# Performance work log

Hardware: AMD Instinct MI355X
Metric: run time of the kernel (lower is better)

The kernel has to match this reference:

```python
import jax, jax.numpy as jnp
import numpy as np


def setup_inputs() -> dict:
    key = jax.random.key(0)
    k1, k2 = jax.random.split(key)
    B, C, H, W = 8, 256, 128, 128
    x = jax.random.normal(k1, (B, C, H, W), dtype=jnp.float32)
    # prior plays the role of torch.rand initial selection score (shape [B, H*W])
    prior = jax.random.uniform(k2, (B, H * W), dtype=jnp.float32)
    return {"x": x, "prior": prior, "nbVec": 16}


def reference(x, prior, nbVec):
    # representativeVectors(x, nbVec, prior=prior, onlySimSample=True, applyUMAP=False)
    B, C, H, W = x.shape
    N = H * W
    xf = x.transpose(0, 2, 3, 1).reshape(B, N, C)  # [B, N, C]
    batch = jnp.arange(B)
    EPS = 1e-12  # numerical guard for sqrt at the selected point (dist == 0)

    def step(carry, i):
        score, selpos = carry  # score: [B, N] selection score, selpos: [B, N]
        # i == 0: deterministic center pick; else data-dependent argmax of score
        ind = jnp.where(i == 0, N // 2, jnp.argmax(score, axis=1))  # [B]
        selpos = selpos.at[batch, ind].add(1.0)
        rv = xf[batch, ind]  # gathered representative candidates [B, C]
        # exp(-euclidean_dist / 20) similarity to every spatial position
        d = jnp.sqrt(jnp.sum((xf - rv[:, None, :]) ** 2, axis=-1) + EPS)  # [B, N]
        sim = jnp.exp(-d / 20.0)
        simNorm = sim / jnp.sum(sim, axis=1, keepdims=True)
        repr_vec = jnp.einsum('bnc,bn->bc', xf, simNorm)  # weighted reduction
        score = jnp.where(i == 0, 1.0 - sim, (1.0 - sim) * score)
        return (score, selpos), (repr_vec, sim)

    init = (prior, jnp.zeros((B, N), dtype=x.dtype))
    (_, selpos), (reprVecs, sims) = jax.lax.scan(step, init, jnp.arange(nbVec))
    # reprVecs: [nbVec, B, C]; sims -> [nbVec, B, 1, H, W]; selpos -> [B, 1, H, W]
    return reprVecs, sims.reshape(nbVec, B, 1, H, W), selpos.reshape(B, 1, H, W)
```

## Files before the change

### kernel.cpp

```cpp
#include <hip/hip_runtime.h>
#include <math.h>

#define BB 8
#define CC 256
#define HH 128
#define WW 128
#define NN (HH*WW)
#define NBVEC 16
#define CSPLIT 16
#define CCHUNK (CC/CSPLIT)
#define NBX (NN/256)
#define NBB 16
#define NSUB 4


__global__ __launch_bounds__(256, 8)
void fused_kernel(const float* __restrict__ x,
                  float* __restrict__ out,
                  const double* __restrict__ bmaxv,
                  const int* __restrict__ bmaxi,
                  float* __restrict__ d2part,
                  double* __restrict__ wpart, int iter)
{
    const int b  = blockIdx.z;
    const int cz = blockIdx.y;
    const int nb = blockIdx.x;
    const int t  = threadIdx.x;

    __shared__ float s_x[CCHUNK][257];
    __shared__ float s_sim[256];
    __shared__ float s_rv[CCHUNK];
    __shared__ union UScratch {
        double part[16][CCHUNK];
        struct { double val[NBX]; int idx[NBX]; } mx;
    } s_u;

    float* out_sims   = out + (size_t)NBVEC*BB*CC;
    float* out_selpos = out_sims + (size_t)NBVEC*BB*NN;

    const float* xb   = x + ((size_t)b*CC + (size_t)cz*CCHUNK)*NN + (size_t)nb*(NSUB*256);
    const float* simb = out_sims + (size_t)(iter-1)*BB*NN + (size_t)b*NN + (size_t)nb*(NSUB*256);
    float r[CCHUNK];
    #pragma unroll
    for (int c = 0; c < CCHUNK; ++c)
        r[c] = xb[(size_t)c*NN + t];
    float simreg = 0.0f;
    if (iter > 0) simreg = simb[t];

    int sel = NN/2;
    if (iter > 0 && iter < NBVEC) {
        if (t < NBX) { s_u.mx.val[t] = bmaxv[b*NBX + t]; s_u.mx.idx[t] = bmaxi[b*NBX + t]; }
        __syncthreads();
        for (int s = NBX/2; s > 0; s >>= 1) {
            if (t < s) {
                double v2 = s_u.mx.val[t+s]; int i2 = s_u.mx.idx[t+s];
                if (v2 > s_u.mx.val[t] || (v2 == s_u.mx.val[t] && i2 < s_u.mx.idx[t])) {
                    s_u.mx.val[t] = v2; s_u.mx.idx[t] = i2;
                }
            }
            __syncthreads();
        }
        sel = s_u.mx.idx[0];
    }

    if (iter < NBVEC) {
        if (t < CCHUNK)
            s_rv[t] = x[((size_t)b*CC + (size_t)cz*CCHUNK + t)*NN + sel];
        if (t == 0 && nb == 0 && cz == 0)
            out_selpos[(size_t)b*NN + sel] += 1.0f;
    }

    for (int sub = 0; sub < NSUB; ++sub) {
        __syncthreads();
        #pragma unroll
        for (int c = 0; c < CCHUNK; ++c)
            s_x[c][t] = r[c];
        if (iter > 0) s_sim[t] = simreg;
        __syncthreads();

        if (sub + 1 < NSUB) {
            const int off = (sub+1)*256;
            #pragma unroll
            for (int c = 0; c < CCHUNK; ++c)
                r[c] = xb[(size_t)c*NN + off + t];
            if (iter > 0) simreg = simb[off + t];
        }

        const int n = nb*(NSUB*256) + sub*256 + t;

        if (iter < NBVEC) {
            double acc = 0.0;
            #pragma unroll
            for (int c = 0; c < CCHUNK; ++c) {
                double diff = (double)s_x[c][t] - (double)s_rv[c];
                acc = fma(diff, diff, acc);
            }
            d2part[((size_t)cz*BB + b)*NN + n] = (float)acc;
        }

        if (iter > 0) {
            const int c = t & 15;
            const int g = t >> 4;
            double w = 0.0;
            #pragma unroll
            for (int k = 0; k < 16; ++k) {
                const int nn2 = g*16 + k;
                w = fma((double)s_sim[nn2], (double)s_x[c][nn2], w);
            }
            s_u.part[g][c] = w;
            __syncthreads();
            if (t < CCHUNK) {
                double t0 = 0.0, t1 = 0.0;
                #pragma unroll
                for (int gg = 0; gg < 16; gg += 2) {
                    t0 += s_u.part[gg][t];
                    t1 += s_u.part[gg+1][t];
                }
                const int nbg = nb*NSUB + sub;
                wpart[((size_t)nbg*BB + b)*CC + (size_t)cz*CCHUNK + t] = t0 + t1;
            }
        }
    }
}

__global__ void finish_kernel(float* __restrict__ out,
                              double* __restrict__ score,
                              const float* __restrict__ d2part,
                              double* __restrict__ sumSim,
                              const double* __restrict__ wpart,
                              double* __restrict__ bmaxv,
                              int* __restrict__ bmaxi, int iter)
{
    const int b = blockIdx.y;
    const int t = threadIdx.x;
    const int n = blockIdx.x * 256 + t;
    const size_t si = (size_t)b*NN + n;
    const int lane = t & 63;
    const int wave = t >> 6;

    double a0 = 0.0, a1 = 0.0;
    #pragma unroll
    for (int cz = 0; cz < CSPLIT; cz += 2) {
        a0 += (double)d2part[((size_t)cz*BB + b)*NN + n];
        a1 += (double)d2part[((size_t)(cz+1)*BB + b)*NN + n];
    }
    double d2 = a0 + a1;

    double d   = sqrt(d2 + 1e-12);
    double sim = exp(-(d / 20.0));

    float* out_sims = out + (size_t)NBVEC*BB*CC;
    out_sims[(size_t)iter*BB*NN + si] = (float)sim;

    double sc;
    if (iter == 0) sc = 1.0 - sim;
    else           sc = (1.0 - sim) * score[si];
    score[si] = sc;

    double v = sim;
    #pragma unroll
    for (int off = 32; off > 0; off >>= 1) v += __shfl_down(v, off, 64);

    double bv = sc; int bi = n;
    #pragma unroll
    for (int off = 32; off > 0; off >>= 1) {
        double ov = __shfl_down(bv, off, 64);
        int    oi = __shfl_down(bi, off, 64);
        if (ov > bv || (ov == bv && oi < bi)) { bv = ov; bi = oi; }
    }

    __shared__ double s_ws[4];
    __shared__ double s_wv[4];
    __shared__ int    s_wi[4];
    if (lane == 0) { s_ws[wave] = v; s_wv[wave] = bv; s_wi[wave] = bi; }
    __syncthreads();
    if (t == 0) {
        double tot = ((s_ws[0] + s_ws[1]) + (s_ws[2] + s_ws[3]));
        atomicAdd(&sumSim[(size_t)(iter & 1)*BB + b], tot);
        double cv = s_wv[0]; int ci = s_wi[0];
        #pragma unroll
        for (int w = 1; w < 4; ++w) {
            if (s_wv[w] > cv || (s_wv[w] == cv && s_wi[w] < ci)) { cv = s_wv[w]; ci = s_wi[w]; }
        }
        bmaxv[(size_t)b*NBX + blockIdx.x] = cv;
        bmaxi[(size_t)b*NBX + blockIdx.x] = ci;
    }

    if (iter > 0 && blockIdx.x == 0) {
        const int slotPrev = (iter-1) & 1;
        double ss = sumSim[(size_t)slotPrev*BB + b];
        if (t < CC) {
            double c0 = 0.0, c1 = 0.0, c2 = 0.0, c3 = 0.0;
            for (int nb = 0; nb < NBX; nb += 4) {
                c0 += wpart[((size_t)(nb+0)*BB + b)*CC + t];
                c1 += wpart[((size_t)(nb+1)*BB + b)*CC + t];
                c2 += wpart[((size_t)(nb+2)*BB + b)*CC + t];
                c3 += wpart[((size_t)(nb+3)*BB + b)*CC + t];
            }
            double tot2 = ((c0 + c1) + (c2 + c3));
            out[(size_t)(iter-1)*BB*CC + (size_t)b*CC + t] = (float)(tot2 / ss);
        }
        __syncthreads();
        if (t == 0) sumSim[(size_t)slotPrev*BB + b] = 0.0;
    }
}

__global__ void final_repr_kernel(float* __restrict__ out,
                                  const double* __restrict__ sumSim,
                                  const double* __restrict__ wpart)
{
    const int b = blockIdx.x;
    const int t = threadIdx.x;
    double ss = sumSim[(size_t)((NBVEC-1) & 1)*BB + b];
    if (t < CC) {
        double c0 = 0.0, c1 = 0.0, c2 = 0.0, c3 = 0.0;
        for (int nb = 0; nb < NBX; nb += 4) {
            c0 += wpart[((size_t)(nb+0)*BB + b)*CC + t];
            c1 += wpart[((size_t)(nb+1)*BB + b)*CC + t];
            c2 += wpart[((size_t)(nb+2)*BB + b)*CC + t];
            c3 += wpart[((size_t)(nb+3)*BB + b)*CC + t];
        }
        double tot = ((c0 + c1) + (c2 + c3));
        out[(size_t)(NBVEC-1)*BB*CC + (size_t)b*CC + t] = (float)(tot / ss);
    }
}

extern "C" void kernel_launch(void* const* d_in, const int* in_sizes, int n_in,
                              void* d_out, int out_size, void* d_ws, size_t ws_size,
                              hipStream_t stream)
{
    const float* x = (const float*)d_in[0];
    float* out = (float*)d_out;

    char* ws = (char*)d_ws;
    double* score  = (double*)(ws);
    float*  d2part = (float*) (ws + 1048576);
    double* wpart  = (double*)(ws + 9437184);
    double* sumSim = (double*)(ws + 10485760);
    double* bmaxv  = (double*)(ws + 10485888);
    int*    bmaxi  = (int*)   (ws + 10489984);

    float* out_selpos = out + (size_t)NBVEC*BB*CC + (size_t)NBVEC*BB*NN;
    hipMemsetAsync(out_selpos, 0, (size_t)BB*NN*sizeof(float), stream);
    hipMemsetAsync(sumSim, 0, 2*BB*sizeof(double), stream);

    for (int i = 0; i <= NBVEC; ++i) {
        fused_kernel<<<dim3(NBB, CSPLIT, BB), 256, 0, stream>>>(
            x, out, bmaxv, bmaxi, d2part, wpart, i);
        if (i < NBVEC)
            finish_kernel<<<dim3(NBX, BB), 256, 0, stream>>>(
                out, score, d2part, sumSim, wpart, bmaxv, bmaxi, i);
    }
    final_repr_kernel<<<BB, 256, 0, stream>>>(out, sumSim, wpart);
}
```

Measured before the change: 840.9 us.

## Accumulate weighted sums in registers per thread, reduce once per block

The fused kernel no longer stages x through shared memory for each sub-tile. Each thread reads its own column values directly, computes the distance in registers, and accumulates sim*x in float registers across all four sub-tiles. A single shared-memory reduction at the end replaces the per-sub-tile one, so wpart shrinks from one partial per 256-column tile to one per block. This cuts shared-memory traffic and barriers, and the finish and final kernels now sum fewer partials. In exchange, the weighted sum is accumulated in float rather than double before the final reduction, which may slightly change precision.

```diff
diff --git a/kernel.cpp b/kernel.cpp
--- a/kernel.cpp
+++ b/kernel.cpp
@@ -27,25 +27,14 @@
     const int nb = blockIdx.x;
     const int t  = threadIdx.x;
 
-    __shared__ float s_x[CCHUNK][257];
-    __shared__ float s_sim[256];
-    __shared__ float s_rv[CCHUNK];
     __shared__ union UScratch {
-        double part[16][CCHUNK];
         struct { double val[NBX]; int idx[NBX]; } mx;
+        float w[CCHUNK][257];
     } s_u;
+    __shared__ double s_part[16][17];
 
     float* out_sims   = out + (size_t)NBVEC*BB*CC;
     float* out_selpos = out_sims + (size_t)NBVEC*BB*NN;
-
-    const float* xb   = x + ((size_t)b*CC + (size_t)cz*CCHUNK)*NN + (size_t)nb*(NSUB*256);
-    const float* simb = out_sims + (size_t)(iter-1)*BB*NN + (size_t)b*NN + (size_t)nb*(NSUB*256);
-    float r[CCHUNK];
-    #pragma unroll
-    for (int c = 0; c < CCHUNK; ++c)
-        r[c] = xb[(size_t)c*NN + t];
-    float simreg = 0.0f;
-    if (iter > 0) simreg = simb[t];
 
     int sel = NN/2;
     if (iter > 0 && iter < NBVEC) {
@@ -63,62 +52,76 @@
         sel = s_u.mx.idx[0];
     }
 
+    if (iter < NBVEC && t == 0 && nb == 0 && cz == 0)
+        out_selpos[(size_t)b*NN + sel] += 1.0f;
+
+    float rvr[CCHUNK];
     if (iter < NBVEC) {
-        if (t < CCHUNK)
-            s_rv[t] = x[((size_t)b*CC + (size_t)cz*CCHUNK + t)*NN + sel];
-        if (t == 0 && nb == 0 && cz == 0)
-            out_selpos[(size_t)b*NN + sel] += 1.0f;
-    }
-
+        const float* rvp = x + ((size_t)b*CC + (size_t)cz*CCHUNK)*NN + sel;
+        #pragma unroll
+        for (int c = 0; c < CCHUNK; ++c)
+            rvr[c] = rvp[(size_t)c*NN];
+    }
+
+    const float* xb   = x + ((size_t)b*CC + (size_t)cz*CCHUNK)*NN + (size_t)nb*(NSUB*256);
+    const float* simb = out_sims + (size_t)(iter-1)*BB*NN + (size_t)b*NN + (size_t)nb*(NSUB*256);
+
+    float wacc[CCHUNK];
+    #pragma unroll
+    for (int c = 0; c < CCHUNK; ++c) wacc[c] = 0.0f;
+
+    #pragma unroll
     for (int sub = 0; sub < NSUB; ++sub) {
-        __syncthreads();
+        float r[CCHUNK];
         #pragma unroll
         for (int c = 0; c < CCHUNK; ++c)
-            s_x[c][t] = r[c];
-        if (iter > 0) s_sim[t] = simreg;
-        __syncthreads();
-
-        if (sub + 1 < NSUB) {
-            const int off = (sub+1)*256;
-            #pragma unroll
-            for (int c = 0; c < CCHUNK; ++c)
-                r[c] = xb[(size_t)c*NN + off + t];
-            if (iter > 0) simreg = simb[off + t];
-        }
-
-        const int n = nb*(NSUB*256) + sub*256 + t;
+            r[c] = xb[(size_t)c*NN + sub*256 + t];
+        float simv = 0.0f;
+        if (iter > 0) simv = simb[sub*256 + t];
 
         if (iter < NBVEC) {
             double acc = 0.0;
             #pragma unroll
             for (int c = 0; c < CCHUNK; ++c) {
-                double diff = (double)s_x[c][t] - (double)s_rv[c];
+                double diff = (double)r[c] - (double)rvr[c];
                 acc = fma(diff, diff, acc);
             }
-            d2part[((size_t)cz*BB + b)*NN + n] = (float)acc;
+            d2part[((size_t)cz*BB + b)*NN + (size_t)nb*(NSUB*256) + sub*256 + t] = (float)acc;
         }
 
         if (iter > 0) {
-            const int c = t & 15;
-            const int g = t >> 4;
-            double w = 0.0;
             #pragma unroll
-            for (int k = 0; k < 16; ++k) {
-                const int nn2 = g*16 + k;
-                w = fma((double)s_sim[nn2], (double)s_x[c][nn2], w);
-            }
-            s_u.part[g][c] = w;
-            __syncthreads();
-            if (t < CCHUNK) {
-                double t0 = 0.0, t1 = 0.0;
-                #pragma unroll
-                for (int gg = 0; gg < 16; gg += 2) {
-                    t0 += s_u.part[gg][t];
-                    t1 += s_u.part[gg+1][t];
-                }
-                const int nbg = nb*NSUB + sub;
-                wpart[((size_t)nbg*BB + b)*CC + (size_t)cz*CCHUNK + t] = t0 + t1;
-            }
+            for (int c = 0; c < CCHUNK; ++c)
+                wacc[c] = fmaf(simv, r[c], wacc[c]);
+        }
+    }
+
+    if (iter > 0) {
+        __syncthreads();
+        #pragma unroll
+        for (int c = 0; c < CCHUNK; ++c)
+            s_u.w[c][t] = wacc[c];
+        __syncthreads();
+        const int c = t & 15;
+        const int g = t >> 4;
+        double t0 = 0.0, t1 = 0.0;
+        #pragma unroll
+        for (int k = 0; k < 16; k += 2) {
+            t0 += (double)s_u.w[c][g*16 + k];
+            t1 += (double)s_u.w[c][g*16 + k + 1];
+        }
+        s_part[g][c] = t0 + t1;
+        __syncthreads();
+        if (t < CCHUNK) {
+            double u0 = 0.0, u1 = 0.0, u2 = 0.0, u3 = 0.0;
+            #pragma unroll
+            for (int gg = 0; gg < 16; gg += 4) {
+                u0 += s_part[gg+0][t];
+                u1 += s_part[gg+1][t];
+                u2 += s_part[gg+2][t];
+                u3 += s_part[gg+3][t];
+            }
+            wpart[((size_t)nb*BB + b)*CC + (size_t)cz*CCHUNK + t] = (u0+u1)+(u2+u3);
         }
     }
 }
@@ -191,7 +194,7 @@
         double ss = sumSim[(size_t)slotPrev*BB + b];
         if (t < CC) {
             double c0 = 0.0, c1 = 0.0, c2 = 0.0, c3 = 0.0;
-            for (int nb = 0; nb < NBX; nb += 4) {
+            for (int nb = 0; nb < NBB; nb += 4) {
                 c0 += wpart[((size_t)(nb+0)*BB + b)*CC + t];
                 c1 += wpart[((size_t)(nb+1)*BB + b)*CC + t];
                 c2 += wpart[((size_t)(nb+2)*BB + b)*CC + t];
@@ -214,7 +217,7 @@
     double ss = sumSim[(size_t)((NBVEC-1) & 1)*BB + b];
     if (t < CC) {
         double c0 = 0.0, c1 = 0.0, c2 = 0.0, c3 = 0.0;
-        for (int nb = 0; nb < NBX; nb += 4) {
+        for (int nb = 0; nb < NBB; nb += 4) {
             c0 += wpart[((size_t)(nb+0)*BB + b)*CC + t];
             c1 += wpart[((size_t)(nb+1)*BB + b)*CC + t];
             c2 += wpart[((size_t)(nb+2)*BB + b)*CC + t];
@@ -236,9 +239,9 @@
     double* score  = (double*)(ws);
     float*  d2part = (float*) (ws + 1048576);
     double* wpart  = (double*)(ws + 9437184);
-    double* sumSim = (double*)(ws + 10485760);
-    double* bmaxv  = (double*)(ws + 10485888);
-    int*    bmaxi  = (int*)   (ws + 10489984);
+    double* sumSim = (double*)(ws + 9699328);
+    double* bmaxv  = (double*)(ws + 9699456);
+    int*    bmaxi  = (int*)   (ws + 9703552);
 
     float* out_selpos = out + (size_t)NBVEC*BB*CC + (size_t)NBVEC*BB*NN;
     hipMemsetAsync(out_selpos, 0, (size_t)BB*NN*sizeof(float), stream);
```

After: 1.187 ms. +41.2%, slower.
